# Optimization experiments

Hardware: AMD Instinct MI355X
Metric: run time of the kernel (lower is better)

The kernel has to match this reference:

```python
import jax, jax.numpy as jnp
import numpy as np
import math

N = 8192
IN_FEATURES = 512
OUT_FEATURES = 512
BUCKET = 4          # self.bucket -> number of hash buckets
NHASH = 1           # nHashTable hardcoded to 1 in forward
NEG = -9e15         # sentinel used by the original module


def setup_inputs() -> dict:
    key = jax.random.key(0)
    k_in, k_adj, k_rot, k_kw, k_vw = jax.random.split(key, 5)
    inp = jax.random.normal(k_in, (N, IN_FEATURES), dtype=jnp.float32)
    adj = jax.random.randint(k_adj, (N, N), 0, 2, dtype=jnp.int32)
    rotations_rands = jax.random.normal(k_rot, (NHASH, OUT_FEATURES, BUCKET // 2), dtype=jnp.float32)
    # xavier_uniform with gain=1.414 for (in, out) matrices
    limit = 1.414 * math.sqrt(6.0 / (IN_FEATURES + OUT_FEATURES))
    kW = jax.random.uniform(k_kw, (IN_FEATURES, OUT_FEATURES), minval=-limit, maxval=limit, dtype=jnp.float32)
    vW = jax.random.uniform(k_vw, (IN_FEATURES, OUT_FEATURES), minval=-limit, maxval=limit, dtype=jnp.float32)
    return {"input": inp, "adj": adj, "rotations_rands": rotations_rands, "kW": kW, "vW": vW}


def reference(input, adj, rotations_rands, kW, vW):
    kh = input @ kW                      # [N, H]
    vh = input @ vW                      # [N, H]
    H = kh.shape[1]

    # LSH bucketing: rotate keys, argmax over [r, -r] -> bucket id per node
    rv = jnp.einsum('nh,thb->tnb', kh, rotations_rands)   # [1, N, B/2]
    rv = jnp.concatenate([rv, -rv], axis=-1)              # [1, N, B]
    buckets = jnp.argmax(rv, axis=2)[0]                   # [N]

    # Original scatters per-bucket kh@kh.T blocks into a dense NxN matrix
    # initialized at NEG; equivalent to masking full scores by same-bucket.
    same_bucket = buckets[:, None] == buckets[None, :]    # [N, N]
    scores = (kh @ kh.T) / jnp.sqrt(jnp.asarray(H, kh.dtype))
    K = jnp.where(same_bucket, scores, NEG)

    attention = jnp.where(adj > 0, K, NEG)
    attention = jax.nn.softmax(attention, axis=1)
    # dropout is identity in eval mode (reference runs in eval)
    h_prime = attention @ vh                              # [N, H]
    return jax.nn.elu(h_prime)                            # concat=True -> ELU
```

## Files before the change

kernel.cpp:

```cpp
#include <hip/hip_runtime.h>
#include <hip/hip_bf16.h>
#include <math.h>

#define N_NODES 8192
#define FEAT 512
#define NEGV -9e15f
#define VHPT_W 8704

typedef __attribute__((ext_vector_type(8))) short short8;
typedef __attribute__((ext_vector_type(4))) float floatx4;

#define OFF_KH    0UL
#define OFF_VH    16777216UL
#define OFF_KHP   33554432UL
#define OFF_VHPT  42074112UL
#define OFF_MASK  50987008UL
#define OFF_S     59375616UL
#define OFF_PERM  109707264UL
#define OFF_FLAGS 109740032UL
#define OFF_BUCK  109772800UL
#define OFF_META  109805568UL
#define OFF_CMEAN 109806592UL
#define WS_NEEDED 109808640UL
#define CAP_S     25165824L

#define OFF_AHI   (OFF_S)
#define OFF_ALO   (OFF_S + 8388608UL)
#define OFF_WKHI  (OFF_S + 16777216UL)
#define OFF_WKLO  (OFF_S + 17301504UL)
#define OFF_WVHI  (OFF_S + 17825792UL)
#define OFF_WVLO  (OFF_S + 18350080UL)
#define OFF_CW    (OFF_MASK)

static __device__ __forceinline__ unsigned short f2bf_bits(float x) {
  __hip_bfloat16 h = __float2bfloat16(x);
  unsigned short u;
  __builtin_memcpy(&u, &h, 2);
  return u;
}
static __device__ __forceinline__ float bf_bits2f(unsigned short u) {
  __hip_bfloat16 h;
  __builtin_memcpy(&h, &u, 2);
  return __bfloat162float(h);
}

__global__ __launch_bounds__(256) void convert_input(
    const float* __restrict__ A, __hip_bfloat16* __restrict__ Ahi,
    __hip_bfloat16* __restrict__ Alo) {
  const long idx = ((long)blockIdx.x * 256 + threadIdx.x) * 4;
  const float4 v = *(const float4*)&A[idx];
  const float vv[4] = {v.x, v.y, v.z, v.w};
  ushort4 hi, lo;
  unsigned short* hp = (unsigned short*)&hi;
  unsigned short* lp = (unsigned short*)&lo;
#pragma unroll
  for (int e = 0; e < 4; e++) {
    unsigned short h = f2bf_bits(vv[e]);
    hp[e] = h;
    lp[e] = f2bf_bits(vv[e] - bf_bits2f(h));
  }
  *(ushort4*)&Ahi[idx] = hi;
  *(ushort4*)&Alo[idx] = lo;
}

__global__ __launch_bounds__(256) void convert_w(
    const float* __restrict__ kW, const float* __restrict__ vW,
    __hip_bfloat16* __restrict__ WkhiT, __hip_bfloat16* __restrict__ WkloT,
    __hip_bfloat16* __restrict__ WvhiT, __hip_bfloat16* __restrict__ WvloT) {
  __shared__ float tile[64][65];
  const int z = blockIdx.z;
  const float* __restrict__ W = z ? vW : kW;
  __hip_bfloat16* __restrict__ HiT = z ? WvhiT : WkhiT;
  __hip_bfloat16* __restrict__ LoT = z ? WvloT : WkloT;
  const int k0 = blockIdx.x * 64, n0 = blockIdx.y * 64;
  const int t = threadIdx.x;
#pragma unroll
  for (int s = 0; s < 16; s++) {
    int idx = t + s * 256;
    int r = idx >> 6, c = idx & 63;
    tile[r][c] = W[(long)(k0 + r) * FEAT + n0 + c];
  }
  __syncthreads();
#pragma unroll
  for (int s = 0; s < 16; s++) {
    int idx = t + s * 256;
    int a = idx >> 6, b = idx & 63;
    float w = tile[b][a];
    unsigned short h = f2bf_bits(w);
    unsigned short l = f2bf_bits(w - bf_bits2f(h));
    __builtin_memcpy(&HiT[(long)(n0 + a) * FEAT + k0 + b], &h, 2);
    __builtin_memcpy(&LoT[(long)(n0 + a) * FEAT + k0 + b], &l, 2);
  }
}

__global__ __launch_bounds__(256) void mfma_dual(
    const __hip_bfloat16* __restrict__ Ahi, const __hip_bfloat16* __restrict__ Alo,
    const __hip_bfloat16* __restrict__ WkhiT, const __hip_bfloat16* __restrict__ WkloT,
    const __hip_bfloat16* __restrict__ WvhiT, const __hip_bfloat16* __restrict__ WvloT,
    float* __restrict__ kh, float* __restrict__ vh) {
  const int z = blockIdx.z;
  const __hip_bfloat16* __restrict__ WhiT = z ? WvhiT : WkhiT;
  const __hip_bfloat16* __restrict__ WloT = z ? WvloT : WkloT;
  float* __restrict__ outp = z ? vh : kh;
  const int ti = blockIdx.x, tj = blockIdx.y;
  __shared__ __align__(16) __hip_bfloat16 Ah[128 * 32];
  __shared__ __align__(16) __hip_bfloat16 Al[128 * 32];
  __shared__ __align__(16) __hip_bfloat16 Wh[128 * 32];
  __shared__ __align__(16) __hip_bfloat16 Wl[128 * 32];
  const int t = threadIdx.x;
  const int lane = t & 63, w = t >> 6;
  const int wm = (w >> 1) * 64, wn = (w & 1) * 64;
  const int quad = lane >> 4, ln = lane & 15;
  const int qr = quad * 8;
  floatx4 acc[4][4];
#pragma unroll
  for (int mi = 0; mi < 4; mi++)
#pragma unroll
    for (int ni = 0; ni < 4; ni++) acc[mi][ni] = (floatx4)0.f;
  for (int k0 = 0; k0 < FEAT; k0 += 32) {
    __syncthreads();
#pragma unroll
    for (int s = 0; s < 2; s++) {
      int c = t + s * 256;
      int row = c >> 2, off8 = (c & 3) * 8;
      *(int4*)&Ah[row * 32 + off8] =
          *(const int4*)&Ahi[(long)(ti * 128 + row) * FEAT + k0 + off8];
      *(int4*)&Al[row * 32 + off8] =
          *(const int4*)&Alo[(long)(ti * 128 + row) * FEAT + k0 + off8];
      *(int4*)&Wh[row * 32 + off8] =
          *(const int4*)&WhiT[(long)(tj * 128 + row) * FEAT + k0 + off8];
      *(int4*)&Wl[row * 32 + off8] =
          *(const int4*)&WloT[(long)(tj * 128 + row) * FEAT + k0 + off8];
    }
    __syncthreads();
    short8 ah[4], al[4], bh[4], bl[4];
#pragma unroll
    for (int mi = 0; mi < 4; mi++) {
      ah[mi] = *(const short8*)&Ah[(wm + mi * 16 + ln) * 32 + qr];
      al[mi] = *(const short8*)&Al[(wm + mi * 16 + ln) * 32 + qr];
    }
#pragma unroll
    for (int ni = 0; ni < 4; ni++) {
      bh[ni] = *(const short8*)&Wh[(wn + ni * 16 + ln) * 32 + qr];
      bl[ni] = *(const short8*)&Wl[(wn + ni * 16 + ln) * 32 + qr];
    }
#pragma unroll
    for (int mi = 0; mi < 4; mi++)
#pragma unroll
      for (int ni = 0; ni < 4; ni++) {
        acc[mi][ni] = __builtin_amdgcn_mfma_f32_16x16x32_bf16(
            ah[mi], bh[ni], acc[mi][ni], 0, 0, 0);
        acc[mi][ni] = __builtin_amdgcn_mfma_f32_16x16x32_bf16(
            ah[mi], bl[ni], acc[mi][ni], 0, 0, 0);
        acc[mi][ni] = __builtin_amdgcn_mfma_f32_16x16x32_bf16(
            al[mi], bh[ni], acc[mi][ni], 0, 0, 0);
      }
  }
#pragma unroll
  for (int mi = 0; mi < 4; mi++)
#pragma unroll
    for (int ni = 0; ni < 4; ni++) {
      int cc = tj * 128 + wn + ni * 16 + ln;
#pragma unroll
      for (int reg = 0; reg < 4; reg++) {
        int r = ti * 128 + wm + mi * 16 + quad * 4 + reg;
        outp[(long)r * FEAT + cc] = acc[mi][ni][reg];
      }
    }
}

__global__ __launch_bounds__(64) void cw_kernel(
    const float* __restrict__ kW, const float* __restrict__ rot,
    double* __restrict__ cw) {
  const int f = blockIdx.x;
  const int lane = threadIdx.x;
  double r0 = 0.0, r1 = 0.0;
  for (int h = lane; h < FEAT; h += 64) {
    double a = (double)kW[(long)f * FEAT + h];
    r0 += a * (double)rot[2 * h];
    r1 += a * (double)rot[2 * h + 1];
  }
#pragma unroll
  for (int off = 32; off > 0; off >>= 1) {
    r0 += __shfl_down(r0, off);
    r1 += __shfl_down(r1, off);
  }
  if (lane == 0) {
    cw[2 * f] = r0;
    cw[2 * f + 1] = r1;
  }
}

__global__ __launch_bounds__(64) void rv_bucket_kernel(
    const float* __restrict__ input, const double* __restrict__ cw,
    int* __restrict__ buckets) {
  const int i = blockIdx.x;
  const int lane = threadIdx.x;
  double r0 = 0.0, r1 = 0.0;
  for (int f = lane; f < FEAT; f += 64) {
    double a = (double)input[(long)i * FEAT + f];
    r0 += a * cw[2 * f];
    r1 += a * cw[2 * f + 1];
  }
#pragma unroll
  for (int off = 32; off > 0; off >>= 1) {
    r0 += __shfl_down(r0, off);
    r1 += __shfl_down(r1, off);
  }
  if (lane == 0) {
    int b = 0;
    double best = r0;
    if (r1 > best)  { best = r1;  b = 1; }
    if (-r0 > best) { best = -r0; b = 2; }
    if (-r1 > best) { best = -r1; b = 3; }
    buckets[i] = b;
  }
}

__global__ __launch_bounds__(256) void sort_kernel(
    const int* __restrict__ buckets, int* __restrict__ perm,
    int* __restrict__ meta) {
  __shared__ int lc[4][256];
  __shared__ int sc[4][256];
  __shared__ int boff_sh[5];
  const int t = threadIdx.x;
  const int base = t * 32;
  int c0 = 0, c1 = 0, c2 = 0, c3 = 0;
  for (int k = 0; k < 32; k++) {
    int b = buckets[base + k];
    c0 += (b == 0); c1 += (b == 1); c2 += (b == 2); c3 += (b == 3);
  }
  lc[0][t] = c0; lc[1][t] = c1; lc[2][t] = c2; lc[3][t] = c3;
  sc[0][t] = c0; sc[1][t] = c1; sc[2][t] = c2; sc[3][t] = c3;
  __syncthreads();
  for (int off = 1; off < 256; off <<= 1) {
    int a0 = (t >= off) ? sc[0][t - off] : 0;
    int a1 = (t >= off) ? sc[1][t - off] : 0;
    int a2 = (t >= off) ? sc[2][t - off] : 0;
    int a3 = (t >= off) ? sc[3][t - off] : 0;
    __syncthreads();
    sc[0][t] += a0; sc[1][t] += a1; sc[2][t] += a2; sc[3][t] += a3;
    __syncthreads();
  }
  if (t == 0) {
    int boff[5];
    boff[0] = 0;
    for (int b = 0; b < 4; b++) boff[b + 1] = boff[b] + sc[b][255];
    for (int b = 0; b < 5; b++) { meta[b] = boff[b]; boff_sh[b] = boff[b]; }
    long so = 0;
    int po = 0;
    for (int b = 0; b < 4; b++) {
      int tot = boff[b + 1] - boff[b];
      int pad = ((tot + 127) >> 7) << 7;
      meta[5 + b] = pad;
      meta[9 + b] = (int)so;
      meta[14 + b] = po;
      so += (long)pad * pad;
      po += pad;
    }
    meta[13] = (int)so;
    meta[18] = po;
    if (so > CAP_S)
      for (int b = 0; b < 4; b++) meta[5 + b] = 0;
  }
  __syncthreads();
  int s0 = boff_sh[0] + sc[0][t] - lc[0][t];
  int s1 = boff_sh[1] + sc[1][t] - lc[1][t];
  int s2 = boff_sh[2] + sc[2][t] - lc[2][t];
  int s3 = boff_sh[3] + sc[3][t] - lc[3][t];
  for (int k = 0; k < 32; k++) {
    int i = base + k;
    int b = buckets[i];
    int pos = (b == 0) ? s0++ : ((b == 1) ? s1++ : ((b == 2) ? s2++ : s3++));
    perm[pos] = i;
  }
}

__global__ __launch_bounds__(256) void gather_khp_kernel(
    const float* __restrict__ kh, const int* __restrict__ perm,
    __hip_bfloat16* __restrict__ khp) {
  const int g = blockIdx.x;
  const int t = threadIdx.x;
  if (g < N_NODES) {
    const int p = perm[g];
    const float2 v = *(const float2*)&kh[(long)p * FEAT + 2 * t];
    khp[(long)g * FEAT + 2 * t] = __float2bfloat16(v.x);
    khp[(long)g * FEAT + 2 * t + 1] = __float2bfloat16(v.y);
  } else {
    khp[(long)g * FEAT + 2 * t] = __float2bfloat16(0.f);
    khp[(long)g * FEAT + 2 * t + 1] = __float2bfloat16(0.f);
  }
}

__global__ __launch_bounds__(256) void transpose_vhpT_kernel(
    const float* __restrict__ vh, const int* __restrict__ perm,
    const int* __restrict__ meta, __hip_bfloat16* __restrict__ vhpT,
    float* __restrict__ cmean) {
  __shared__ float tile[64][65];
  __shared__ float cred[4][64];
  const int g0 = blockIdx.x * 64;
  const int f0 = blockIdx.y * 64;
  const int t = threadIdx.x;
#pragma unroll
  for (int s = 0; s < 16; s++) {
    int idx = t + s * 256;
    int r = idx >> 6, c = idx & 63;
    int pos = g0 + r;
    int b = (pos >= meta[15]) + (pos >= meta[16]) + (pos >= meta[17]);
    int local = pos - meta[14 + b];
    int n_b = meta[b + 1] - meta[b];
    float v = 0.f;
    if (local < n_b) v = vh[(long)perm[meta[b] + local] * FEAT + f0 + c];
    tile[r][c] = v;
  }
  __syncthreads();
  {
    const int c = t & 63, seg = t >> 6;
    float ps = 0.f;
#pragma unroll
    for (int rr = 0; rr < 16; rr++) ps += tile[seg * 16 + rr][c];
    cred[seg][c] = ps;
  }
  __syncthreads();
  if (t < 64)
    atomicAdd(&cmean[f0 + t],
              cred[0][t] + cred[1][t] + cred[2][t] + cred[3][t]);
#pragma unroll
  for (int s = 0; s < 16; s++) {
    int idx = t + s * 256;
    int fr = idx >> 6, gc = idx & 63;
    vhpT[(long)(f0 + fr) * VHPT_W + g0 + gc] = __float2bfloat16(tile[gc][fr]);
  }
}

__global__ __launch_bounds__(256) void maskpack_kernel(
    const int* __restrict__ adj, const int* __restrict__ perm,
    const int* __restrict__ meta, unsigned long long* __restrict__ maskbits) {
  __shared__ int adj_lds[N_NODES];
  const int g = blockIdx.x;
  const int t = threadIdx.x;
  const int b = (g >= meta[1]) + (g >= meta[2]) + (g >= meta[3]);
  const int boff = meta[b];
  const int n_b = meta[b + 1] - boff;
  const int padded = meta[5 + b];
  const int i = perm[g];
  const int* arow = adj + (long)i * N_NODES;
#pragma unroll
  for (int s = 0; s < 8; s++) {
    int idx = (t + s * 256) * 4;
    *(int4*)&adj_lds[idx] = *(const int4*)&arow[idx];
  }
  __syncthreads();
  const int lane = t & 63, w = t >> 6;
  for (int jj0 = w * 64; jj0 < padded; jj0 += 256) {
    int jj = jj0 + lane;
    int pred = 0;
    if (jj < n_b) pred = adj_lds[perm[boff + jj]] > 0;
    unsigned long long mword = __ballot(pred);
    if (lane == 0) maskbits[(long)g * 128 + (jj0 >> 6)] = mword;
  }
}

__global__ __launch_bounds__(256) void s_gemm(
    const __hip_bfloat16* __restrict__ khp, const int* __restrict__ meta,
    const unsigned long long* __restrict__ maskbits,
    __hip_bfloat16* __restrict__ S) {
  const int b = blockIdx.z;
  const int padded = meta[5 + b];
  const int ti = blockIdx.x, tj = blockIdx.y;
  if (ti * 128 >= padded || tj * 128 >= padded) return;
  const int boff = meta[b];
  const long soff = meta[9 + b];
  __shared__ __align__(16) __hip_bfloat16 As[128 * 32];
  __shared__ __align__(16) __hip_bfloat16 Bs[128 * 32];
  const int t = threadIdx.x;
  const int lane = t & 63, w = t >> 6;
  const int wm = (w >> 1) * 64, wn = (w & 1) * 64;
  const int quad = lane >> 4, ln = lane & 15;
  const int qr = quad * 8;
  floatx4 acc[4][4];
#pragma unroll
  for (int mi = 0; mi < 4; mi++)
#pragma unroll
    for (int ni = 0; ni < 4; ni++) acc[mi][ni] = (floatx4)0.f;
  const long a_g0 = boff + ti * 128;
  const long b_g0 = boff + tj * 128;
  for (int k0 = 0; k0 < FEAT; k0 += 32) {
    __syncthreads();
#pragma unroll
    for (int s = 0; s < 2; s++) {
      int c = t + s * 256;
      int row = c >> 2, off8 = (c & 3) * 8;
      *(int4*)&As[row * 32 + off8] =
          *(const int4*)&khp[(a_g0 + row) * FEAT + k0 + off8];
      *(int4*)&Bs[row * 32 + off8] =
          *(const int4*)&khp[(b_g0 + row) * FEAT + k0 + off8];
    }
    __syncthreads();
    short8 af[4], bfr[4];
#pragma unroll
    for (int mi = 0; mi < 4; mi++)
      af[mi] = *(const short8*)&As[(wm + mi * 16 + ln) * 32 + qr];
#pragma unroll
    for (int ni = 0; ni < 4; ni++)
      bfr[ni] = *(const short8*)&Bs[(wn + ni * 16 + ln) * 32 + qr];
#pragma unroll
    for (int mi = 0; mi < 4; mi++)
#pragma unroll
      for (int ni = 0; ni < 4; ni++)
        acc[mi][ni] = __builtin_amdgcn_mfma_f32_16x16x32_bf16(
            af[mi], bfr[ni], acc[mi][ni], 0, 0, 0);
  }
  const float scale = 0.04419417382415922f;
#pragma unroll
  for (int mi = 0; mi < 4; mi++) {
#pragma unroll
    for (int ni = 0; ni < 4; ni++) {
      int cb = tj * 128 + wn + ni * 16;
#pragma unroll
      for (int reg = 0; reg < 4; reg++) {
        int r = ti * 128 + wm + mi * 16 + quad * 4 + reg;
        unsigned long long wbits = maskbits[(long)(boff + r) * 128 + (cb >> 6)];
        int bit = (int)((wbits >> ((cb & 63) + ln)) & 1ULL);
        float v = acc[mi][ni][reg] * scale;
        S[soff + (long)r * padded + cb + ln] =
            __float2bfloat16(bit ? v : NEGV);
      }
    }
  }
}

__global__ __launch_bounds__(256) void softmax_kernel(
    __hip_bfloat16* __restrict__ S, const int* __restrict__ meta,
    int* __restrict__ flags) {
  const int g = blockIdx.x;
  const int b = (g >= meta[1]) + (g >= meta[2]) + (g >= meta[3]);
  const int boff = meta[b];
  const int padded = meta[5 + b];
  const long soff = meta[9 + b];
  __hip_bfloat16* row = S + soff + (long)(g - boff) * padded;
  __shared__ float red[256];
  __shared__ float pb[8192];
  const int t = threadIdx.x;
  float m = -INFINITY;
  for (int j0 = t * 8; j0 < padded; j0 += 2048) {
    union { short8 v; unsigned short u[8]; } pk;
    pk.v = *(const short8*)&row[j0];
#pragma unroll
    for (int e = 0; e < 8; e++) {
      float s = bf_bits2f(pk.u[e]);
      pb[j0 + e] = s;
      m = fmaxf(m, s);
    }
  }
  red[t] = m;
  __syncthreads();
#pragma unroll
  for (int o = 128; o > 0; o >>= 1) {
    if (t < o) red[t] = fmaxf(red[t], red[t + o]);
    __syncthreads();
  }
  m = red[0];
  __syncthreads();
  if (m < -8e15f) {
    if (t == 0) flags[g] = 1;
    union { short8 v; unsigned short u[8]; } zz;
#pragma unroll
    for (int e = 0; e < 8; e++) zz.u[e] = 0;
    for (int j0 = t * 8; j0 < padded; j0 += 2048) *(short8*)&row[j0] = zz.v;
    return;
  }
  if (t == 0) flags[g] = 0;
  float sum = 0.f;
  for (int j0 = t * 8; j0 < padded; j0 += 2048) {
#pragma unroll
    for (int e = 0; e < 8; e++) {
      float ex = expf(pb[j0 + e] - m);
      pb[j0 + e] = ex;
      sum += ex;
    }
  }
  red[t] = sum;
  __syncthreads();
#pragma unroll
  for (int o = 128; o > 0; o >>= 1) {
    if (t < o) red[t] += red[t + o];
    __syncthreads();
  }
  const float inv = 1.f / red[0];
  for (int j0 = t * 8; j0 < padded; j0 += 2048) {
    union { short8 v; unsigned short u[8]; } pk;
#pragma unroll
    for (int e = 0; e < 8; e++) pk.u[e] = f2bf_bits(pb[j0 + e] * inv);
    *(short8*)&row[j0] = pk.v;
  }
}

__global__ __launch_bounds__(256) void pv_gemm(
    const __hip_bfloat16* __restrict__ S, const __hip_bfloat16* __restrict__ vhpT,
    const int* __restrict__ meta, const int* __restrict__ perm,
    const int* __restrict__ flags, const float* __restrict__ cmean,
    float* __restrict__ out) {
  const int b = blockIdx.z;
  const int padded = meta[5 + b];
  const int ti = blockIdx.x;
  if (ti * 128 >= padded) return;
  const int boff = meta[b];
  const int n_b = meta[b + 1] - boff;
  const long soff = meta[9 + b];
  const int poff = meta[14 + b];
  const int f0 = blockIdx.y * 64;
  __shared__ __align__(16) __hip_bfloat16 As[128 * 32];
  __shared__ __align__(16) __hip_bfloat16 Bs[64 * 32];
  const int t = threadIdx.x;
  const int lane = t & 63, w = t >> 6;
  const int wm = w * 32;
  const int quad = lane >> 4, ln = lane & 15;
  const int qr = quad * 8;
  floatx4 acc[2][4];
#pragma unroll
  for (int mi = 0; mi < 2; mi++)
#pragma unroll
    for (int ni = 0; ni < 4; ni++) acc[mi][ni] = (floatx4)0.f;
  const long r0 = (long)ti * 128;
  for (int k0 = 0; k0 < padded; k0 += 32) {
    __syncthreads();
#pragma unroll
    for (int s = 0; s < 2; s++) {
      int c = t + s * 256;
      int row = c >> 2, off8 = (c & 3) * 8;
      *(int4*)&As[row * 32 + off8] =
          *(const int4*)&S[soff + (r0 + row) * padded + k0 + off8];
    }
    {
      int row = t >> 2, off8 = (t & 3) * 8;
      *(int4*)&Bs[row * 32 + off8] =
          *(const int4*)&vhpT[(long)(f0 + row) * VHPT_W + poff + k0 + off8];
    }
    __syncthreads();
    short8 af[2], bfr[4];
#pragma unroll
    for (int mi = 0; mi < 2; mi++)
      af[mi] = *(const short8*)&As[(wm + mi * 16 + ln) * 32 + qr];
#pragma unroll
    for (int ni = 0; ni < 4; ni++)
      bfr[ni] = *(const short8*)&Bs[(ni * 16 + ln) * 32 + qr];
#pragma unroll
    for (int mi = 0; mi < 2; mi++)
#pragma unroll
      for (int ni = 0; ni < 4; ni++)
        acc[mi][ni] = __builtin_amdgcn_mfma_f32_16x16x32_bf16(
            af[mi], bfr[ni], acc[mi][ni], 0, 0, 0);
  }
#pragma unroll
  for (int mi = 0; mi < 2; mi++) {
#pragma unroll
    for (int reg = 0; reg < 4; reg++) {
      int r = ti * 128 + wm + mi * 16 + quad * 4 + reg;
      if (r < n_b) {
        int g = boff + r;
        int node = perm[g];
        int fl = flags[g];
#pragma unroll
        for (int ni = 0; ni < 4; ni++) {
          int fc = f0 + ni * 16 + ln;
          float v = fl ? cmean[fc] * (1.f / (float)N_NODES)
                       : acc[mi][ni][reg];
          v = v > 0.f ? v : expm1f(v);
          out[(long)node * FEAT + fc] = v;
        }
      }
    }
  }
}

__global__ __launch_bounds__(256) void gemm_dual(
    const float* __restrict__ A, const float* __restrict__ Wk,
    const float* __restrict__ Wv, float* __restrict__ kh,
    float* __restrict__ vh) {
  __shared__ float As[32][33];
  __shared__ float Bk[32][33];
  __shared__ float Bv[32][33];
  const int tid = threadIdx.x;
  const int row0 = blockIdx.x * 32;
  const int col0 = blockIdx.y * 32;
  const int tx = tid & 15, ty = tid >> 4;
  float ck00 = 0.f, ck01 = 0.f, ck10 = 0.f, ck11 = 0.f;
  float cv00 = 0.f, cv01 = 0.f, cv10 = 0.f, cv11 = 0.f;
  for (int kt = 0; kt < FEAT; kt += 32) {
#pragma unroll
    for (int t = 0; t < 4; t++) {
      int e = tid + t * 256;
      int r = e >> 5, c = e & 31;
      As[r][c] = A[(long)(row0 + r) * FEAT + kt + c];
      Bk[r][c] = Wk[(long)(kt + r) * FEAT + col0 + c];
      Bv[r][c] = Wv[(long)(kt + r) * FEAT + col0 + c];
    }
    __syncthreads();
#pragma unroll
    for (int kk = 0; kk < 32; kk++) {
      float a0 = As[ty * 2][kk], a1 = As[ty * 2 + 1][kk];
      float bk0 = Bk[kk][tx * 2], bk1 = Bk[kk][tx * 2 + 1];
      float bv0 = Bv[kk][tx * 2], bv1 = Bv[kk][tx * 2 + 1];
      ck00 += a0 * bk0; ck01 += a0 * bk1;
      ck10 += a1 * bk0; ck11 += a1 * bk1;
      cv00 += a0 * bv0; cv01 += a0 * bv1;
      cv10 += a1 * bv0; cv11 += a1 * bv1;
    }
    __syncthreads();
  }
  const int r0 = row0 + ty * 2, c0 = col0 + tx * 2;
  kh[(long)r0 * FEAT + c0] = ck00;       kh[(long)r0 * FEAT + c0 + 1] = ck01;
  kh[(long)(r0 + 1) * FEAT + c0] = ck10; kh[(long)(r0 + 1) * FEAT + c0 + 1] = ck11;
  vh[(long)r0 * FEAT + c0] = cv00;       vh[(long)r0 * FEAT + c0 + 1] = cv01;
  vh[(long)(r0 + 1) * FEAT + c0] = cv10; vh[(long)(r0 + 1) * FEAT + c0 + 1] = cv11;
}

__global__ __launch_bounds__(64) void bucket_kernel(
    const float* __restrict__ kh, const float* __restrict__ rot,
    int* __restrict__ buckets) {
  const int i = blockIdx.x;
  const int lane = threadIdx.x;
  double r0 = 0.0, r1 = 0.0;
  for (int h = lane; h < FEAT; h += 64) {
    double a = (double)kh[(long)i * FEAT + h];
    r0 += a * (double)rot[2 * h];
    r1 += a * (double)rot[2 * h + 1];
  }
#pragma unroll
  for (int off = 32; off > 0; off >>= 1) {
    r0 += __shfl_down(r0, off);
    r1 += __shfl_down(r1, off);
  }
  if (lane == 0) {
    int b = 0;
    double best = r0;
    if (r1 > best)  { best = r1;  b = 1; }
    if (-r0 > best) { best = -r0; b = 2; }
    if (-r1 > best) { best = -r1; b = 3; }
    buckets[i] = b;
  }
}

__global__ __launch_bounds__(256) void attn_kernel(
    const float* __restrict__ kh, const float* __restrict__ vh,
    const int* __restrict__ adj, const int* __restrict__ buckets,
    float* __restrict__ out) {
  __shared__ float khi[FEAT];
  __shared__ float pbuf[N_NODES];
  __shared__ unsigned short jlist[N_NODES];
  __shared__ int cnt_sh;
  __shared__ float red[256];
  const int i = blockIdx.x;
  const int tid = threadIdx.x;
  if (tid == 0) cnt_sh = 0;
  for (int k = tid; k < FEAT; k += 256) khi[k] = kh[(long)i * FEAT + k];
  const int mybucket = buckets[i];
  __syncthreads();
  const int* adjrow = adj + (long)i * N_NODES;
  for (int j = tid; j < N_NODES; j += 256) {
    if (adjrow[j] > 0 && buckets[j] == mybucket) {
      int idx = atomicAdd(&cnt_sh, 1);
      jlist[idx] = (unsigned short)j;
    }
  }
  __syncthreads();
  const int cnt = cnt_sh;
  float mloc = -INFINITY;
  for (int idx = tid; idx < cnt; idx += 256) {
    int j = jlist[idx];
    const float4* kj = (const float4*)(kh + (long)j * FEAT);
    const float4* ki = (const float4*)khi;
    float acc = 0.f;
#pragma unroll 8
    for (int k = 0; k < FEAT / 4; k++) {
      float4 a = ki[k];
      float4 b = kj[k];
      acc += a.x * b.x + a.y * b.y + a.z * b.z + a.w * b.w;
    }
    float s = acc * 0.04419417382415922f;
    pbuf[idx] = s;
    mloc = fmaxf(mloc, s);
  }
  red[tid] = mloc;
  __syncthreads();
#pragma unroll
  for (int off = 128; off > 0; off >>= 1) {
    if (tid < off) red[tid] = fmaxf(red[tid], red[tid + off]);
    __syncthreads();
  }
  const float m = red[0];
  __syncthreads();
  float lloc = 0.f;
  for (int idx = tid; idx < cnt; idx += 256) {
    float p = expf(pbuf[idx] - m);
    pbuf[idx] = p;
    lloc += p;
  }
  red[tid] = lloc;
  __syncthreads();
#pragma unroll
  for (int off = 128; off > 0; off >>= 1) {
    if (tid < off) red[tid] += red[tid + off];
    __syncthreads();
  }
  const float l = red[0];
  __syncthreads();
  const int f = 2 * tid;
  float acc0 = 0.f, acc1 = 0.f;
  if (cnt > 0) {
#pragma unroll 4
    for (int idx = 0; idx < cnt; idx++) {
      int j = jlist[idx];
      float p = pbuf[idx];
      float2 v = *(const float2*)(vh + (long)j * FEAT + f);
      acc0 += p * v.x;
      acc1 += p * v.y;
    }
    float invl = 1.f / l;
    acc0 *= invl;
    acc1 *= invl;
  } else {
    for (int j = 0; j < N_NODES; j++) {
      float2 v = *(const float2*)(vh + (long)j * FEAT + f);
      acc0 += v.x;
      acc1 += v.y;
    }
    acc0 *= (1.f / (float)N_NODES);
    acc1 *= (1.f / (float)N_NODES);
  }
  acc0 = acc0 > 0.f ? acc0 : expm1f(acc0);
  acc1 = acc1 > 0.f ? acc1 : expm1f(acc1);
  *(float2*)(out + (long)i * FEAT + f) = make_float2(acc0, acc1);
}

extern "C" void kernel_launch(void* const* d_in, const int* in_sizes, int n_in,
                              void* d_out, int out_size, void* d_ws,
                              size_t ws_size, hipStream_t stream) {
  const float* input = (const float*)d_in[0];
  const int* adj = (const int*)d_in[1];
  const float* rot = (const float*)d_in[2];
  const float* kW = (const float*)d_in[3];
  const float* vW = (const float*)d_in[4];
  float* out = (float*)d_out;

  char* ws = (char*)d_ws;
  float* kh = (float*)(ws + OFF_KH);
  float* vh = (float*)(ws + OFF_VH);

  if (ws_size >= WS_NEEDED) {
    __hip_bfloat16* khp = (__hip_bfloat16*)(ws + OFF_KHP);
    __hip_bfloat16* vhpT = (__hip_bfloat16*)(ws + OFF_VHPT);
    unsigned long long* maskbits = (unsigned long long*)(ws + OFF_MASK);
    __hip_bfloat16* S = (__hip_bfloat16*)(ws + OFF_S);
    int* perm = (int*)(ws + OFF_PERM);
    int* flags = (int*)(ws + OFF_FLAGS);
    int* buckets = (int*)(ws + OFF_BUCK);
    int* meta = (int*)(ws + OFF_META);
    float* cmean = (float*)(ws + OFF_CMEAN);
    __hip_bfloat16* Ahi = (__hip_bfloat16*)(ws + OFF_AHI);
    __hip_bfloat16* Alo = (__hip_bfloat16*)(ws + OFF_ALO);
    __hip_bfloat16* WkhiT = (__hip_bfloat16*)(ws + OFF_WKHI);
    __hip_bfloat16* WkloT = (__hip_bfloat16*)(ws + OFF_WKLO);
    __hip_bfloat16* WvhiT = (__hip_bfloat16*)(ws + OFF_WVHI);
    __hip_bfloat16* WvloT = (__hip_bfloat16*)(ws + OFF_WVLO);
    double* cw = (double*)(ws + OFF_CW);

    convert_input<<<4096, 256, 0, stream>>>(input, Ahi, Alo);
    convert_w<<<dim3(8, 8, 2), 256, 0, stream>>>(kW, vW, WkhiT, WkloT, WvhiT,
                                                 WvloT);
    mfma_dual<<<dim3(64, 4, 2), 256, 0, stream>>>(Ahi, Alo, WkhiT, WkloT,
                                                  WvhiT, WvloT, kh, vh);
    cw_kernel<<<512, 64, 0, stream>>>(kW, rot, cw);
    rv_bucket_kernel<<<N_NODES, 64, 0, stream>>>(input, cw, buckets);
    sort_kernel<<<1, 256, 0, stream>>>(buckets, perm, meta);
    gather_khp_kernel<<<N_NODES + 128, 256, 0, stream>>>(kh, perm, khp);
    hipMemsetAsync(cmean, 0, FEAT * sizeof(float), stream);
    transpose_vhpT_kernel<<<dim3(VHPT_W / 64, FEAT / 64), 256, 0, stream>>>(
        vh, perm, meta, vhpT, cmean);
    maskpack_kernel<<<N_NODES, 256, 0, stream>>>(adj, perm, meta, maskbits);
    s_gemm<<<dim3(64, 64, 4), 256, 0, stream>>>(khp, meta, maskbits, S);
    softmax_kernel<<<N_NODES, 256, 0, stream>>>(S, meta, flags);
    pv_gemm<<<dim3(64, 8, 4), 256, 0, stream>>>(S, vhpT, meta, perm, flags,
                                                cmean, out);
  } else {
    dim3 gemm_grid(N_NODES / 32, FEAT / 32);
    gemm_dual<<<gemm_grid, 256, 0, stream>>>(input, kW, vW, kh, vh);
    int* buckets = (int*)(vh + (long)N_NODES * FEAT);
    bucket_kernel<<<N_NODES, 64, 0, stream>>>(kh, rot, buckets);
    attn_kernel<<<N_NODES, 256, 0, stream>>>(kh, vh, adj, buckets, out);
  }
}
```

Baseline: 662.5 us.

## Fuse softmax into score GEMM using Cauchy-Schwarz row bound and deferred normalisation

Drops the standalone softmax pass. s_gemm now writes exp(score - bound) directly, where the bound is the row key norm times the bucket's maximum key norm, which upper-bounds each dot product by Cauchy-Schwarz. It also emits per-tile partial row sums, a small reduce kernel turns them into inverse sums, and pv_gemm applies that normalisation. The projection GEMM writes bf16 output already scattered into bucket order through an inverse permutation, which removes the fp32 kh/vh buffers and the gather kernel; maskpack now computes the empty-row flags. The cost is extra norm and reduce kernels, and a risk of exp underflow when the bound is far above the true row max.

```diff
diff --git a/kernel.cpp b/kernel.cpp
--- a/kernel.cpp
+++ b/kernel.cpp
@@ -10,19 +10,24 @@
 typedef __attribute__((ext_vector_type(8))) short short8;
 typedef __attribute__((ext_vector_type(4))) float floatx4;
 
-#define OFF_KH    0UL
-#define OFF_VH    16777216UL
-#define OFF_KHP   33554432UL
-#define OFF_VHPT  42074112UL
-#define OFF_MASK  50987008UL
-#define OFF_S     59375616UL
-#define OFF_PERM  109707264UL
-#define OFF_FLAGS 109740032UL
-#define OFF_BUCK  109772800UL
-#define OFF_META  109805568UL
-#define OFF_CMEAN 109806592UL
-#define WS_NEEDED 109808640UL
-#define CAP_S     25165824L
+#define OFF_VHB   0UL
+#define OFF_KHP   8388608UL
+#define OFF_VHPT  16908288UL
+#define OFF_MASK  25821184UL
+#define OFF_ST    34340864UL
+#define OFF_LINV  38797312UL
+#define OFF_NORMK 38832128UL
+#define OFF_MAXN  38865408UL
+#define OFF_PERM  38865664UL
+#define OFF_INVP  38898432UL
+#define OFF_FLAGS 38931200UL
+#define OFF_BUCK  38963968UL
+#define OFF_META  38996736UL
+#define OFF_CMEAN 38996864UL
+#define OFF_CW    38998912UL
+#define OFF_S     39007104UL
+#define WS_NEEDED 181613440UL
+#define CAP_S     71303168L
 
 #define OFF_AHI   (OFF_S)
 #define OFF_ALO   (OFF_S + 8388608UL)
@@ -30,7 +35,6 @@
 #define OFF_WKLO  (OFF_S + 17301504UL)
 #define OFF_WVHI  (OFF_S + 17825792UL)
 #define OFF_WVLO  (OFF_S + 18350080UL)
-#define OFF_CW    (OFF_MASK)
 
 static __device__ __forceinline__ unsigned short f2bf_bits(float x) {
   __hip_bfloat16 h = __float2bfloat16(x);
@@ -97,11 +101,12 @@
     const __hip_bfloat16* __restrict__ Ahi, const __hip_bfloat16* __restrict__ Alo,
     const __hip_bfloat16* __restrict__ WkhiT, const __hip_bfloat16* __restrict__ WkloT,
     const __hip_bfloat16* __restrict__ WvhiT, const __hip_bfloat16* __restrict__ WvloT,
-    float* __restrict__ kh, float* __restrict__ vh) {
+    const int* __restrict__ invp, __hip_bfloat16* __restrict__ khp,
+    __hip_bfloat16* __restrict__ vhb) {
   const int z = blockIdx.z;
   const __hip_bfloat16* __restrict__ WhiT = z ? WvhiT : WkhiT;
   const __hip_bfloat16* __restrict__ WloT = z ? WvloT : WkloT;
-  float* __restrict__ outp = z ? vh : kh;
+  __hip_bfloat16* __restrict__ outp = z ? vhb : khp;
   const int ti = blockIdx.x, tj = blockIdx.y;
   __shared__ __align__(16) __hip_bfloat16 Ah[128 * 32];
   __shared__ __align__(16) __hip_bfloat16 Al[128 * 32];
@@ -159,12 +164,13 @@
 #pragma unroll
   for (int mi = 0; mi < 4; mi++)
 #pragma unroll
-    for (int ni = 0; ni < 4; ni++) {
-      int cc = tj * 128 + wn + ni * 16 + ln;
-#pragma unroll
-      for (int reg = 0; reg < 4; reg++) {
-        int r = ti * 128 + wm + mi * 16 + quad * 4 + reg;
-        outp[(long)r * FEAT + cc] = acc[mi][ni][reg];
+    for (int reg = 0; reg < 4; reg++) {
+      const int node = ti * 128 + wm + mi * 16 + quad * 4 + reg;
+      const long dst = z ? node : invp[node];
+#pragma unroll
+      for (int ni = 0; ni < 4; ni++) {
+        int cc = tj * 128 + wn + ni * 16 + ln;
+        outp[dst * FEAT + cc] = __float2bfloat16(acc[mi][ni][reg]);
       }
     }
 }
@@ -219,7 +225,7 @@
 
 __global__ __launch_bounds__(256) void sort_kernel(
     const int* __restrict__ buckets, int* __restrict__ perm,
-    int* __restrict__ meta) {
+    int* __restrict__ invp, int* __restrict__ meta) {
   __shared__ int lc[4][256];
   __shared__ int sc[4][256];
   __shared__ int boff_sh[5];
@@ -273,27 +279,37 @@
     int b = buckets[i];
     int pos = (b == 0) ? s0++ : ((b == 1) ? s1++ : ((b == 2) ? s2++ : s3++));
     perm[pos] = i;
-  }
-}
-
-__global__ __launch_bounds__(256) void gather_khp_kernel(
-    const float* __restrict__ kh, const int* __restrict__ perm,
-    __hip_bfloat16* __restrict__ khp) {
+    invp[i] = pos;
+  }
+}
+
+__global__ __launch_bounds__(64) void normk_kernel(
+    const __hip_bfloat16* __restrict__ khp, const int* __restrict__ meta,
+    float* __restrict__ normk, float* __restrict__ maxn) {
   const int g = blockIdx.x;
-  const int t = threadIdx.x;
-  if (g < N_NODES) {
-    const int p = perm[g];
-    const float2 v = *(const float2*)&kh[(long)p * FEAT + 2 * t];
-    khp[(long)g * FEAT + 2 * t] = __float2bfloat16(v.x);
-    khp[(long)g * FEAT + 2 * t + 1] = __float2bfloat16(v.y);
-  } else {
-    khp[(long)g * FEAT + 2 * t] = __float2bfloat16(0.f);
-    khp[(long)g * FEAT + 2 * t + 1] = __float2bfloat16(0.f);
+  const int lane = threadIdx.x;
+  union { int4 v; unsigned short u[8]; } pk;
+  pk.v = *(const int4*)&khp[(long)g * FEAT + lane * 8];
+  float s = 0.f;
+#pragma unroll
+  for (int e = 0; e < 8; e++) {
+    float x = bf_bits2f(pk.u[e]);
+    s += x * x;
+  }
+#pragma unroll
+  for (int off = 32; off > 0; off >>= 1) s += __shfl_xor(s, off);
+  if (lane == 0) {
+    float n = sqrtf(s);
+    normk[g] = n;
+    if (g < N_NODES) {
+      int b = (g >= meta[1]) + (g >= meta[2]) + (g >= meta[3]);
+      atomicMax((int*)&maxn[b], __float_as_int(n));
+    }
   }
 }
 
 __global__ __launch_bounds__(256) void transpose_vhpT_kernel(
-    const float* __restrict__ vh, const int* __restrict__ perm,
+    const __hip_bfloat16* __restrict__ vhb, const int* __restrict__ perm,
     const int* __restrict__ meta, __hip_bfloat16* __restrict__ vhpT,
     float* __restrict__ cmean) {
   __shared__ float tile[64][65];
@@ -310,7 +326,8 @@
     int local = pos - meta[14 + b];
     int n_b = meta[b + 1] - meta[b];
     float v = 0.f;
-    if (local < n_b) v = vh[(long)perm[meta[b] + local] * FEAT + f0 + c];
+    if (local < n_b)
+      v = __bfloat162float(vhb[(long)perm[meta[b] + local] * FEAT + f0 + c]);
     tile[r][c] = v;
   }
   __syncthreads();
@@ -335,10 +352,13 @@
 
 __global__ __launch_bounds__(256) void maskpack_kernel(
     const int* __restrict__ adj, const int* __restrict__ perm,
-    const int* __restrict__ meta, unsigned long long* __restrict__ maskbits) {
+    const int* __restrict__ meta, unsigned long long* __restrict__ maskbits,
+    int* __restrict__ flags) {
   __shared__ int adj_lds[N_NODES];
+  __shared__ int any_sh;
   const int g = blockIdx.x;
   const int t = threadIdx.x;
+  if (t == 0) any_sh = 0;
   const int b = (g >= meta[1]) + (g >= meta[2]) + (g >= meta[3]);
   const int boff = meta[b];
   const int n_b = meta[b + 1] - boff;
@@ -357,19 +377,26 @@
     int pred = 0;
     if (jj < n_b) pred = adj_lds[perm[boff + jj]] > 0;
     unsigned long long mword = __ballot(pred);
-    if (lane == 0) maskbits[(long)g * 128 + (jj0 >> 6)] = mword;
-  }
+    if (lane == 0) {
+      maskbits[(long)g * 128 + (jj0 >> 6)] = mword;
+      if (mword) any_sh = 1;
+    }
+  }
+  __syncthreads();
+  if (t == 0) flags[g] = any_sh ? 0 : 1;
 }
 
 __global__ __launch_bounds__(256) void s_gemm(
     const __hip_bfloat16* __restrict__ khp, const int* __restrict__ meta,
     const unsigned long long* __restrict__ maskbits,
-    __hip_bfloat16* __restrict__ S) {
+    const float* __restrict__ normk, const float* __restrict__ maxn,
+    __hip_bfloat16* __restrict__ S, float* __restrict__ st) {
   const int b = blockIdx.z;
   const int padded = meta[5 + b];
   const int ti = blockIdx.x, tj = blockIdx.y;
   if (ti * 128 >= padded || tj * 128 >= padded) return;
   const int boff = meta[b];
+  const int poff = meta[14 + b];
   const long soff = meta[9 + b];
   __shared__ __align__(16) __hip_bfloat16 As[128 * 32];
   __shared__ __align__(16) __hip_bfloat16 Bs[128 * 32];
@@ -412,95 +439,53 @@
             af[mi], bfr[ni], acc[mi][ni], 0, 0, 0);
   }
   const float scale = 0.04419417382415922f;
+  const float maxnb = maxn[b];
 #pragma unroll
   for (int mi = 0; mi < 4; mi++) {
 #pragma unroll
-    for (int ni = 0; ni < 4; ni++) {
-      int cb = tj * 128 + wn + ni * 16;
-#pragma unroll
-      for (int reg = 0; reg < 4; reg++) {
-        int r = ti * 128 + wm + mi * 16 + quad * 4 + reg;
+    for (int reg = 0; reg < 4; reg++) {
+      const int r = ti * 128 + wm + mi * 16 + quad * 4 + reg;
+      const float bnd = normk[boff + r] * maxnb * scale;
+      float rowsum = 0.f;
+#pragma unroll
+      for (int ni = 0; ni < 4; ni++) {
+        const int cb = tj * 128 + wn + ni * 16;
         unsigned long long wbits = maskbits[(long)(boff + r) * 128 + (cb >> 6)];
         int bit = (int)((wbits >> ((cb & 63) + ln)) & 1ULL);
-        float v = acc[mi][ni][reg] * scale;
-        S[soff + (long)r * padded + cb + ln] =
-            __float2bfloat16(bit ? v : NEGV);
+        float p = bit ? expf(acc[mi][ni][reg] * scale - bnd) : 0.f;
+        S[soff + (long)r * padded + cb + ln] = __float2bfloat16(p);
+        rowsum += p;
       }
-    }
-  }
-}
-
-__global__ __launch_bounds__(256) void softmax_kernel(
-    __hip_bfloat16* __restrict__ S, const int* __restrict__ meta,
-    int* __restrict__ flags) {
-  const int g = blockIdx.x;
-  const int b = (g >= meta[1]) + (g >= meta[2]) + (g >= meta[3]);
-  const int boff = meta[b];
-  const int padded = meta[5 + b];
-  const long soff = meta[9 + b];
-  __hip_bfloat16* row = S + soff + (long)(g - boff) * padded;
-  __shared__ float red[256];
-  __shared__ float pb[8192];
-  const int t = threadIdx.x;
-  float m = -INFINITY;
-  for (int j0 = t * 8; j0 < padded; j0 += 2048) {
-    union { short8 v; unsigned short u[8]; } pk;
-    pk.v = *(const short8*)&row[j0];
-#pragma unroll
-    for (int e = 0; e < 8; e++) {
-      float s = bf_bits2f(pk.u[e]);
-      pb[j0 + e] = s;
-      m = fmaxf(m, s);
-    }
-  }
-  red[t] = m;
-  __syncthreads();
-#pragma unroll
-  for (int o = 128; o > 0; o >>= 1) {
-    if (t < o) red[t] = fmaxf(red[t], red[t + o]);
-    __syncthreads();
-  }
-  m = red[0];
-  __syncthreads();
-  if (m < -8e15f) {
-    if (t == 0) flags[g] = 1;
-    union { short8 v; unsigned short u[8]; } zz;
-#pragma unroll
-    for (int e = 0; e < 8; e++) zz.u[e] = 0;
-    for (int j0 = t * 8; j0 < padded; j0 += 2048) *(short8*)&row[j0] = zz.v;
-    return;
-  }
-  if (t == 0) flags[g] = 0;
-  float sum = 0.f;
-  for (int j0 = t * 8; j0 < padded; j0 += 2048) {
-#pragma unroll
-    for (int e = 0; e < 8; e++) {
-      float ex = expf(pb[j0 + e] - m);
-      pb[j0 + e] = ex;
-      sum += ex;
-    }
-  }
-  red[t] = sum;
-  __syncthreads();
-#pragma unroll
-  for (int o = 128; o > 0; o >>= 1) {
-    if (t < o) red[t] += red[t + o];
-    __syncthreads();
-  }
-  const float inv = 1.f / red[0];
-  for (int j0 = t * 8; j0 < padded; j0 += 2048) {
-    union { short8 v; unsigned short u[8]; } pk;
-#pragma unroll
-    for (int e = 0; e < 8; e++) pk.u[e] = f2bf_bits(pb[j0 + e] * inv);
-    *(short8*)&row[j0] = pk.v;
-  }
+      rowsum += __shfl_xor(rowsum, 1);
+      rowsum += __shfl_xor(rowsum, 2);
+      rowsum += __shfl_xor(rowsum, 4);
+      rowsum += __shfl_xor(rowsum, 8);
+      if (ln == 0)
+        st[(long)(poff + r) * 128 + tj * 2 + (wn >> 6)] = rowsum;
+    }
+  }
+}
+
+__global__ __launch_bounds__(64) void reduce_kernel(
+    const float* __restrict__ st, const int* __restrict__ meta,
+    float* __restrict__ linv) {
+  const int prow = blockIdx.x;
+  if (prow >= meta[18]) return;
+  const int b = (prow >= meta[15]) + (prow >= meta[16]) + (prow >= meta[17]);
+  const int ntiles = meta[5 + b] >> 6;
+  const int lane = threadIdx.x;
+  float s = 0.f;
+  for (int j = lane; j < ntiles; j += 64) s += st[(long)prow * 128 + j];
+#pragma unroll
+  for (int off = 32; off > 0; off >>= 1) s += __shfl_xor(s, off);
+  if (lane == 0) linv[prow] = s > 0.f ? 1.f / s : 0.f;
 }
 
 __global__ __launch_bounds__(256) void pv_gemm(
     const __hip_bfloat16* __restrict__ S, const __hip_bfloat16* __restrict__ vhpT,
     const int* __restrict__ meta, const int* __restrict__ perm,
-    const int* __restrict__ flags, const float* __restrict__ cmean,
-    float* __restrict__ out) {
+    const int* __restrict__ flags, const float* __restrict__ linv,
+    const float* __restrict__ cmean, float* __restrict__ out) {
   const int b = blockIdx.z;
   const int padded = meta[5 + b];
   const int ti = blockIdx.x;
@@ -561,11 +546,12 @@
         int g = boff + r;
         int node = perm[g];
         int fl = flags[g];
+        float li = linv[poff + r];
 #pragma unroll
         for (int ni = 0; ni < 4; ni++) {
           int fc = f0 + ni * 16 + ln;
           float v = fl ? cmean[fc] * (1.f / (float)N_NODES)
-                       : acc[mi][ni][reg];
+                       : acc[mi][ni][reg] * li;
           v = v > 0.f ? v : expm1f(v);
           out[(long)node * FEAT + fc] = v;
         }
@@ -745,48 +731,59 @@
   float* out = (float*)d_out;
 
   char* ws = (char*)d_ws;
-  float* kh = (float*)(ws + OFF_KH);
-  float* vh = (float*)(ws + OFF_VH);
 
   if (ws_size >= WS_NEEDED) {
+    __hip_bfloat16* vhb = (__hip_bfloat16*)(ws + OFF_VHB);
     __hip_bfloat16* khp = (__hip_bfloat16*)(ws + OFF_KHP);
     __hip_bfloat16* vhpT = (__hip_bfloat16*)(ws + OFF_VHPT);
     unsigned long long* maskbits = (unsigned long long*)(ws + OFF_MASK);
-    __hip_bfloat16* S = (__hip_bfloat16*)(ws + OFF_S);
+    float* st = (float*)(ws + OFF_ST);
+    float* linv = (float*)(ws + OFF_LINV);
+    float* normk = (float*)(ws + OFF_NORMK);
+    float* maxn = (float*)(ws + OFF_MAXN);
     int* perm = (int*)(ws + OFF_PERM);
+    int* invp = (int*)(ws + OFF_INVP);
     int* flags = (int*)(ws + OFF_FLAGS);
     int* buckets = (int*)(ws + OFF_BUCK);
     int* meta = (int*)(ws + OFF_META);
     float* cmean = (float*)(ws + OFF_CMEAN);
+    double* cw = (double*)(ws + OFF_CW);
+    __hip_bfloat16* S = (__hip_bfloat16*)(ws + OFF_S);
     __hip_bfloat16* Ahi = (__hip_bfloat16*)(ws + OFF_AHI);
     __hip_bfloat16* Alo = (__hip_bfloat16*)(ws + OFF_ALO);
     __hip_bfloat16* WkhiT = (__hip_bfloat16*)(ws + OFF_WKHI);
     __hip_bfloat16* WkloT = (__hip_bfloat16*)(ws + OFF_WKLO);
     __hip_bfloat16* WvhiT = (__hip_bfloat16*)(ws + OFF_WVHI);
     __hip_bfloat16* WvloT = (__hip_bfloat16*)(ws + OFF_WVLO);
-    double* cw = (double*)(ws + OFF_CW);
-
+
+    cw_kernel<<<512, 64, 0, stream>>>(kW, rot, cw);
+    rv_bucket_kernel<<<N_NODES, 64, 0, stream>>>(input, cw, buckets);
+    sort_kernel<<<1, 256, 0, stream>>>(buckets, perm, invp, meta);
     convert_input<<<4096, 256, 0, stream>>>(input, Ahi, Alo);
     convert_w<<<dim3(8, 8, 2), 256, 0, stream>>>(kW, vW, WkhiT, WkloT, WvhiT,
                                                  WvloT);
+    hipMemsetAsync(khp + (long)N_NODES * FEAT, 0, 128 * FEAT * 2, stream);
     mfma_dual<<<dim3(64, 4, 2), 256, 0, stream>>>(Ahi, Alo, WkhiT, WkloT,
-                                                  WvhiT, WvloT, kh, vh);
-    cw_kernel<<<512, 64, 0, stream>>>(kW, rot, cw);
-    rv_bucket_kernel<<<N_NODES, 64, 0, stream>>>(input, cw, buckets);
-    sort_kernel<<<1, 256, 0, stream>>>(buckets, perm, meta);
-    gather_khp_kernel<<<N_NODES + 128, 256, 0, stream>>>(kh, perm, khp);
+                                                  WvhiT, WvloT, invp, khp,
+                                                  vhb);
+    hipMemsetAsync(maxn, 0, 16, stream);
+    normk_kernel<<<8320, 64, 0, stream>>>(khp, meta, normk, maxn);
     hipMemsetAsync(cmean, 0, FEAT * sizeof(float), stream);
     transpose_vhpT_kernel<<<dim3(VHPT_W / 64, FEAT / 64), 256, 0, stream>>>(
-        vh, perm, meta, vhpT, cmean);
-    maskpack_kernel<<<N_NODES, 256, 0, stream>>>(adj, perm, meta, maskbits);
-    s_gemm<<<dim3(64, 64, 4), 256, 0, stream>>>(khp, meta, maskbits, S);
-    softmax_kernel<<<N_NODES, 256, 0, stream>>>(S, meta, flags);
+        vhb, perm, meta, vhpT, cmean);
+    maskpack_kernel<<<N_NODES, 256, 0, stream>>>(adj, perm, meta, maskbits,
+                                                 flags);
+    s_gemm<<<dim3(64, 64, 4), 256, 0, stream>>>(khp, meta, maskbits, normk,
+                                                maxn, S, st);
+    reduce_kernel<<<8704, 64, 0, stream>>>(st, meta, linv);
     pv_gemm<<<dim3(64, 8, 4), 256, 0, stream>>>(S, vhpT, meta, perm, flags,
-                                                cmean, out);
+                                                linv, cmean, out);
   } else {
+    float* kh = (float*)(ws + 0UL);
+    float* vh = (float*)(ws + 16777216UL);
+    int* buckets = (int*)(ws + 33554432UL);
     dim3 gemm_grid(N_NODES / 32, FEAT / 32);
     gemm_dual<<<gemm_grid, 256, 0, stream>>>(input, kW, vW, kh, vh);
-    int* buckets = (int*)(vh + (long)N_NODES * FEAT);
     bucket_kernel<<<N_NODES, 64, 0, stream>>>(kh, rot, buckets);
     attn_kernel<<<N_NODES, 256, 0, stream>>>(kh, vh, adj, buckets, out);
   }
```

New measurement: 764.4 us. 15.4% more time.
